# Optimization experiments

Hardware: AMD Instinct MI355X
Metric: run time of the kernel (lower is better)

## Reference

```python
import jax, jax.numpy as jnp
import numpy as np
import math

B, C, D, H, W = 1, 64, 16, 16, 16
HEADS = 4
HD = C // HEADS  # head_dim = 16


def conv3d(x, w, b, pad):
    # x: [B,C,D,H,W], w: [O,I,kd,kh,kw], pad: (pd,ph,pw)
    y = jax.lax.conv_general_dilated(
        x, w, window_strides=(1, 1, 1),
        padding=[(p, p) for p in pad],
        dimension_numbers=('NCDHW', 'OIDHW', 'NCDHW'))
    return y + b[None, :, None, None, None]


def setup_inputs() -> dict:
    key = jax.random.key(0)
    ks = jax.random.split(key, 10)
    s = 0.02
    return {
        'x': jax.random.normal(ks[0], (B, C, D, H, W), jnp.float32),
        'gamma': jax.random.normal(ks[1], (1,), jnp.float32),
        'w_sp': jax.random.normal(ks[2], (C, C, 1, 3, 3), jnp.float32) * s,
        'b_sp': jax.random.normal(ks[3], (C,), jnp.float32) * s,
        'w_spec': jax.random.normal(ks[4], (C, C, 3, 1, 1), jnp.float32) * s,
        'b_spec': jax.random.normal(ks[5], (C,), jnp.float32) * s,
        'w_qkv': jax.random.normal(ks[6], (3 * C, C, 1, 1, 1), jnp.float32) * s,
        'b_qkv': jax.random.normal(ks[7], (3 * C,), jnp.float32) * s,
        'w_proj': jax.random.normal(ks[8], (C, C, 1, 1, 1), jnp.float32) * s,
        'b_proj': jax.random.normal(ks[9], (C,), jnp.float32) * s,
    }


def _decay_exponent(dtype):
    # Faithful to the torch permute quirk (requires H == W):
    # exponent[i,j,k,m,n,o] = |i-m| + |j-k| + |n-o|
    dd = jnp.abs(jnp.arange(D)[:, None] - jnp.arange(D)[None, :]).astype(dtype)  # [D,D]
    hh = jnp.abs(jnp.arange(H)[:, None] - jnp.arange(H)[None, :]).astype(dtype)  # [H,H]
    ww = jnp.abs(jnp.arange(W)[:, None] - jnp.arange(W)[None, :]).astype(dtype)  # [W,W]
    return (dd[:, None, None, :, None, None]      # i (axis0), m (axis3)
            + hh[None, :, :, None, None, None]    # j (axis1), k (axis2)
            + ww[None, None, None, None, :, :])   # n (axis4), o (axis5)


def _forward(x, gamma, w_sp, b_sp, w_spec, b_spec, w_qkv, b_qkv, w_proj, b_proj):
    x = conv3d(x, w_sp, b_sp, (0, 1, 1))
    x = conv3d(x, w_spec, b_spec, (1, 0, 0))
    qkv = conv3d(x, w_qkv, b_qkv, (0, 0, 0))
    q, k, v = jnp.split(qkv, 3, axis=1)
    rs = lambda t: t.reshape(B, HEADS, HD, D, H, W)
    q, k, v = rs(q), rs(k), rs(v)

    g = jax.nn.sigmoid(gamma[0])
    decay = g ** _decay_exponent(x.dtype)  # [D,H,W,D,W,W] (H==W)

    # attn[b,h,i,j,k,m,n,o]: (i,j,k)=query D,H,W ; (m,n,o)=key D,H,W
    attn = jnp.einsum('bhdijk,bhdmno->bhijkmno', q, k) / math.sqrt(HD)
    attn = jax.nn.softmax(attn * decay, axis=-1)  # softmax over key-W axis o only
    out = jnp.einsum('bhijkmno,bhdmno->bhdijk', attn, v)
    out = out.reshape(B, C, D, H, W)
    return conv3d(out, w_proj, b_proj, (0, 0, 0))


def reference(x, gamma, w_sp, b_sp, w_spec, b_spec, w_qkv, b_qkv, w_proj, b_proj):
    return _forward(x, gamma, w_sp, b_sp, w_spec, b_spec, w_qkv, b_qkv, w_proj, b_proj)
```

## Files before the change

### kernel.cpp

```cpp
#include <hip/hip_runtime.h>
#include <math.h>

#define CN   262144
#define BTP 196
#define PTP 68

typedef __attribute__((ext_vector_type(8))) short short8;
typedef __attribute__((ext_vector_type(4))) short short4v;
typedef __attribute__((ext_vector_type(4))) float float4v;

static __device__ __forceinline__ unsigned short f2bf(float f) {
    union { float f; unsigned u; } v; v.f = f;
    unsigned r = (v.u + 0x7FFFu + ((v.u >> 16) & 1u)) >> 16;
    return (unsigned short)r;
}

__global__ __launch_bounds__(512) void wprep_kernel(
        const float* __restrict__ w_sp,
        const float* __restrict__ w_spec, const float* __restrict__ b_spec,
        const float* __restrict__ w_qkv, const float* __restrict__ b_qkv,
        unsigned short* __restrict__ wsb,
        unsigned short* __restrict__ wfb, float* __restrict__ bfv) {
    int idx = blockIdx.x * 512 + threadIdx.x;
    if (idx < 36864) {
        int dh  = idx / 12288;
        int rem = idx % 12288;
        int co  = rem / 192;
        int kp  = rem % 192;
        int ci = kp / 3, dw = kp % 3;
        wsb[idx] = f2bf(w_sp[co * 576 + ci * 9 + dh * 3 + dw]);
    } else {
        int j = idx - 36864;
        int oc = j / 192;
        int r  = j % 192;
        float s = 0.f;
        #pragma unroll 8
        for (int ci = 0; ci < 64; ++ci)
            s += w_qkv[oc * 64 + ci] * w_spec[ci * 192 + r];
        if (oc < 64) s *= 0.25f;
        wfb[oc * 192 + r] = f2bf(s);
        if (j < 192) {
            float t = b_qkv[j];
            for (int ci = 0; ci < 64; ++ci) t += w_qkv[j * 64 + ci] * b_spec[ci];
            if (j < 64) t *= 0.25f;
            bfv[j] = t;
        }
    }
}

__global__ __launch_bounds__(256, 4) void conv_sp_mfma_kernel(
        const float* __restrict__ x, const unsigned short* __restrict__ wsb,
        const float* __restrict__ b_sp, float* __restrict__ y1) {
    __shared__ __align__(16) unsigned short Bt[16 * BTP];
    int d = blockIdx.x >> 4;
    int h = blockIdx.x & 15;
    int tid = threadIdx.x;
    int px = tid & 15, cig = tid >> 4;

    float rcur[12], rnxt[12];
    #define LOAD_CHUNK(dh_, rr)                                            \
        {                                                                  \
            int hh = h + (dh_) - 1;                                        \
            _Pragma("unroll")                                              \
            for (int cc = 0; cc < 4; ++cc) {                               \
                int ci = cig * 4 + cc;                                     \
                const float* xr = x + ci * 4096 + d * 256 + hh * 16;       \
                _Pragma("unroll")                                          \
                for (int dw = 0; dw < 3; ++dw) {                           \
                    int ww = px + dw - 1;                                  \
                    float v = 0.f;                                         \
                    if (hh >= 0 && hh <= 15 && ww >= 0 && ww <= 15)        \
                        v = xr[ww];                                        \
                    (rr)[cc * 3 + dw] = v;                                 \
                }                                                          \
            }                                                              \
        }

    LOAD_CHUNK(0, rcur);

    int wv = tid >> 6, lane = tid & 63;
    int quad = lane >> 4, l15 = lane & 15;
    float4v czero = {0.f, 0.f, 0.f, 0.f};
    float4v acc = czero;

    #pragma unroll
    for (int c = 0; c < 3; ++c) {
        __syncthreads();
        #pragma unroll
        for (int cc = 0; cc < 4; ++cc) {
            int ci = cig * 4 + cc;
            Bt[px * BTP + ci * 3 + 0] = f2bf(rcur[cc * 3 + 0]);
            Bt[px * BTP + ci * 3 + 1] = f2bf(rcur[cc * 3 + 1]);
            Bt[px * BTP + ci * 3 + 2] = f2bf(rcur[cc * 3 + 2]);
        }
        __syncthreads();
        if (c < 2) LOAD_CHUNK(c + 1, rnxt);

        const unsigned short* ab = wsb + c * 12288 + (wv * 16 + l15) * 192 + quad * 8;
        const unsigned short* brow = Bt + l15 * BTP + quad * 8;
        #pragma unroll
        for (int ks = 0; ks < 6; ++ks) {
            short8 af = *(const short8*)(ab + ks * 32);
            short4v lo = *(const short4v*)(brow + ks * 32);
            short4v hi = *(const short4v*)(brow + ks * 32 + 4);
            short8 bf8 = {lo[0], lo[1], lo[2], lo[3], hi[0], hi[1], hi[2], hi[3]};
            acc = __builtin_amdgcn_mfma_f32_16x16x32_bf16(af, bf8, acc, 0, 0, 0);
        }
        #pragma unroll
        for (int q2 = 0; q2 < 12; ++q2) rcur[q2] = rnxt[q2];
    }

    int p = d * 256 + h * 16 + l15;
    #pragma unroll
    for (int r = 0; r < 4; ++r) {
        int co = wv * 16 + quad * 4 + r;
        y1[co * 4096 + p] = acc[r] + b_sp[co];
    }
    #undef LOAD_CHUNK
}

__global__ __launch_bounds__(512, 4) void qkv_mfma_kernel(
        const float* __restrict__ y1, const unsigned short* __restrict__ wfb,
        const float* __restrict__ bfv,
        unsigned short* __restrict__ qb, unsigned short* __restrict__ kb,
        unsigned short* __restrict__ vtb) {
    __shared__ __align__(16) unsigned short Bt[32 * BTP];
    int bI  = blockIdx.x;
    int ocg = bI % 3;
    int pq  = (bI / 3) & 7;
    int d   = bI / 24;
    int tid = threadIdx.x;

    {
        int px  = tid & 31;
        int cig = tid >> 5;
        const float* yb = y1 + d * 256 + pq * 32 + px;
        #pragma unroll
        for (int cc = 0; cc < 4; ++cc) {
            int ci = cig * 4 + cc;
            const float* yc = yb + ci * 4096;
            #pragma unroll
            for (int t = 0; t < 3; ++t) {
                float v = 0.f;
                if (!((d == 0 && t == 0) || (d == 15 && t == 2)))
                    v = yc[(t - 1) * 256];
                Bt[px * BTP + ci * 3 + t] = f2bf(v);
            }
        }
    }

    int wv = tid >> 6, lane = tid & 63;
    int quad = lane >> 4, l15 = lane & 15;
    int Mt = wv >> 1;
    int nt = wv & 1;

    short8 af[6];
    {
        const unsigned short* ab = wfb + (ocg * 64 + Mt * 16 + l15) * 192 + quad * 8;
        #pragma unroll
        for (int ks = 0; ks < 6; ++ks) af[ks] = *(const short8*)(ab + ks * 32);
    }
    float bias[4];
    #pragma unroll
    for (int r = 0; r < 4; ++r) bias[r] = bfv[ocg * 64 + Mt * 16 + quad * 4 + r];

    __syncthreads();

    float4v czero = {0.f, 0.f, 0.f, 0.f};
    float4v acc = czero;
    {
        const unsigned short* brow = Bt + (nt * 16 + l15) * BTP + quad * 8;
        #pragma unroll
        for (int ks = 0; ks < 6; ++ks) {
            short4v lo = *(const short4v*)(brow + ks * 32);
            short4v hi = *(const short4v*)(brow + ks * 32 + 4);
            short8 bf8 = {lo[0], lo[1], lo[2], lo[3], hi[0], hi[1], hi[2], hi[3]};
            acc = __builtin_amdgcn_mfma_f32_16x16x32_bf16(af[ks], bf8, acc, 0, 0, 0);
        }
    }

    {
        int p = d * 256 + pq * 32 + nt * 16 + l15;
        if (ocg == 2) {
            int h = (p >> 4) & 15, w0 = p & 15;
            int kap = 8 * (w0 >> 2) + 4 * (h & 1) + (w0 & 3);
            unsigned short* dst = vtb + ((Mt * 16 + d) * 8 + (h >> 1)) * 512
                                      + (quad * 4) * 32 + kap;
            #pragma unroll
            for (int r = 0; r < 4; ++r) dst[r * 32] = f2bf(acc[r] + bias[r]);
        } else {
            unsigned short* dst = (ocg == 0 ? qb : kb) + Mt * 65536 + p * 16 + quad * 4;
            unsigned t0 = (unsigned)f2bf(acc[0] + bias[0])
                        | ((unsigned)f2bf(acc[1] + bias[1]) << 16);
            unsigned t1 = (unsigned)f2bf(acc[2] + bias[2])
                        | ((unsigned)f2bf(acc[3] + bias[3]) << 16);
            *(unsigned*)dst = t0;
            *(unsigned*)(dst + 2) = t1;
        }
    }
}

__global__ __launch_bounds__(512, 4) void attn_kernel(
        const unsigned short* __restrict__ qb, const unsigned short* __restrict__ kb,
        const unsigned short* __restrict__ vtb, const float* __restrict__ gamma,
        float* __restrict__ aoall) {
    __shared__ __align__(16) unsigned short ksh[2][4096];
    __shared__ __align__(16) unsigned short vsh[2][4096];
    __shared__ float gp[32];
    int tid = threadIdx.x;
    int bI = blockIdx.x;
    int head = bI >> 8;
    int mg   = (bI >> 5) & 7;
    int oct  = bI & 31;

    if (tid < 32) {
        float g = 1.f / (1.f + __expf(-gamma[0]));
        gp[tid] = __powf(g, (float)tid);
    }

    int wv = tid >> 6, lane = tid & 63;
    int quad = lane >> 4, l15 = lane & 15;
    int t = oct * 8 + wv;
    int i = t >> 4, j = t & 15;

    short8 zero8 = {0, 0, 0, 0, 0, 0, 0, 0};
    float4v czero = {0.f, 0.f, 0.f, 0.f};
    short8 qf = zero8;
    if (quad < 2)
        qf = *(const short8*)(qb + head * 65536 + (t * 16 + l15) * 16 + quad * 8);

    const unsigned short* kbh = kb  + head * 65536 + mg * 2 * 4096;
    const unsigned short* vbh = vtb + head * 65536 + mg * 2 * 4096;
    float4 k0 = ((const float4*)kbh)[tid];
    float4 v0 = ((const float4*)vbh)[tid];
    float4 k1 = ((const float4*)(kbh + 4096))[tid];
    float4 v1 = ((const float4*)(vbh + 4096))[tid];
    ((float4*)ksh[0])[tid] = k0;
    ((float4*)vsh[0])[tid] = v0;
    ((float4*)ksh[1])[tid] = k1;
    ((float4*)vsh[1])[tid] = v1;
    __syncthreads();

    float wd[4];
    #pragma unroll
    for (int r = 0; r < 4; ++r)
        wd[r] = gp[abs(l15 - (quad * 4 + r))] * 1.4426950408889634f;

    float4v O = czero;
    #pragma unroll
    for (int mm = 0; mm < 2; ++mm) {
        int m = mg * 2 + mm;
        const unsigned short* kk = ksh[mm];
        const unsigned short* vv = vsh[mm];
        int eim = abs(i - m);
        #pragma unroll
        for (int np = 0; np < 8; ++np) {
            union { unsigned u[4]; short8 s8; } a2u;
            #pragma unroll
            for (int s = 0; s < 2; ++s) {
                int n = np * 2 + s;
                short8 a1 = zero8;
                if (quad < 2)
                    a1 = *(const short8*)(kk + n * 256 + l15 * 16 + quad * 8);
                float4v d1 = __builtin_amdgcn_mfma_f32_16x16x32_bf16(a1, qf, czero, 0, 0, 0);
                float smn = gp[eim + abs(j - n)];
                float e0 = __builtin_amdgcn_exp2f(d1[0] * smn * wd[0]);
                float e1 = __builtin_amdgcn_exp2f(d1[1] * smn * wd[1]);
                float e2 = __builtin_amdgcn_exp2f(d1[2] * smn * wd[2]);
                float e3 = __builtin_amdgcn_exp2f(d1[3] * smn * wd[3]);
                float sm = e0 + e1 + e2 + e3;
                sm += __shfl_xor(sm, 16);
                sm += __shfl_xor(sm, 32);
                float inv = __builtin_amdgcn_rcpf(sm);
                union { float f; unsigned u; } p0, p1, p2, p3;
                p0.f = e0 * inv; p1.f = e1 * inv;
                p2.f = e2 * inv; p3.f = e3 * inv;
                a2u.u[s * 2]     = ((p0.u + 0x8000u) >> 16) | ((p1.u + 0x8000u) & 0xFFFF0000u);
                a2u.u[s * 2 + 1] = ((p2.u + 0x8000u) >> 16) | ((p3.u + 0x8000u) & 0xFFFF0000u);
            }
            short8 b2 = *(const short8*)(vv + np * 512 + l15 * 32 + quad * 8);
            O = __builtin_amdgcn_mfma_f32_16x16x32_bf16(a2u.s8, b2, O, 0, 0, 0);
        }
    }

    float* aop = aoall + mg * CN;
    float4 ov = {O[0], O[1], O[2], O[3]};
    *(float4*)(aop + (head * 16 + l15) * 4096 + t * 16 + quad * 4) = ov;
}

__global__ __launch_bounds__(256, 8) void proj_mfma_kernel(
        const float* __restrict__ aoall,
        const float* __restrict__ w, const float* __restrict__ b,
        float* __restrict__ out) {
    __shared__ __align__(16) unsigned short Bt[16 * PTP];
    int d   = blockIdx.x >> 4;
    int p16 = blockIdx.x & 15;
    int tid = threadIdx.x;

    {
        int px = tid & 15, cig = tid >> 4;
        int gbase = d * 256 + p16 * 16 + px;
        #pragma unroll
        for (int cc = 0; cc < 4; ++cc) {
            int ci = cig * 4 + cc;
            int ga = ci * 4096 + gbase;
            float v = 0.f;
            #pragma unroll
            for (int k = 0; k < 8; ++k) v += aoall[k * CN + ga];
            Bt[px * PTP + ci] = f2bf(v);
        }
    }
    __syncthreads();

    int wv = tid >> 6, lane = tid & 63;
    int quad = lane >> 4, l15 = lane & 15;
    float4v czero = {0.f, 0.f, 0.f, 0.f};
    float4v acc = czero;

    short8 af[2];
    const float* wsrc = w + (wv * 16 + l15) * 64 + quad * 8;
    #pragma unroll
    for (int ks = 0; ks < 2; ++ks) {
        float4 wa = *(const float4*)(wsrc + ks * 32);
        float4 wb = *(const float4*)(wsrc + ks * 32 + 4);
        short8 a8 = {(short)f2bf(wa.x), (short)f2bf(wa.y), (short)f2bf(wa.z),
                     (short)f2bf(wa.w), (short)f2bf(wb.x), (short)f2bf(wb.y),
                     (short)f2bf(wb.z), (short)f2bf(wb.w)};
        af[ks] = a8;
    }
    const unsigned short* brow = Bt + l15 * PTP + quad * 8;
    #pragma unroll
    for (int ks = 0; ks < 2; ++ks) {
        short4v lo = *(const short4v*)(brow + ks * 32);
        short4v hi = *(const short4v*)(brow + ks * 32 + 4);
        short8 bf8 = {lo[0], lo[1], lo[2], lo[3], hi[0], hi[1], hi[2], hi[3]};
        acc = __builtin_amdgcn_mfma_f32_16x16x32_bf16(af[ks], bf8, acc, 0, 0, 0);
    }

    int p = d * 256 + p16 * 16 + l15;
    #pragma unroll
    for (int r = 0; r < 4; ++r) {
        int oc = wv * 16 + quad * 4 + r;
        out[oc * 4096 + p] = acc[r] + b[oc];
    }
}

extern "C" void kernel_launch(void* const* d_in, const int* in_sizes, int n_in,
                              void* d_out, int out_size, void* d_ws, size_t ws_size,
                              hipStream_t stream) {
    const float* x      = (const float*)d_in[0];
    const float* gamma  = (const float*)d_in[1];
    const float* w_sp   = (const float*)d_in[2];
    const float* b_sp   = (const float*)d_in[3];
    const float* w_spec = (const float*)d_in[4];
    const float* b_spec = (const float*)d_in[5];
    const float* w_qkv  = (const float*)d_in[6];
    const float* b_qkv  = (const float*)d_in[7];
    const float* w_proj = (const float*)d_in[8];
    const float* b_proj = (const float*)d_in[9];
    float* out = (float*)d_out;

    float* ws = (float*)d_ws;
    float* y1  = ws;
    unsigned short* wfb = (unsigned short*)(ws + CN);
    float* bfv = ws + CN + 20480;
    unsigned short* wsb = (unsigned short*)(ws + CN + 24576);
    unsigned short* qb  = (unsigned short*)(ws + 2 * CN);
    unsigned short* kb  = (unsigned short*)(ws + 2 * CN + CN / 2);
    unsigned short* vtb = (unsigned short*)(ws + 3 * CN);
    float* aoall = ws + 3 * CN + CN / 2;

    wprep_kernel       <<< 144, 512, 0, stream>>>(w_sp, w_spec, b_spec,
                                                  w_qkv, b_qkv, wsb, wfb, bfv);
    conv_sp_mfma_kernel<<< 256, 256, 0, stream>>>(x, wsb, b_sp, y1);
    qkv_mfma_kernel    <<< 384, 512, 0, stream>>>(y1, wfb, bfv, qb, kb, vtb);
    attn_kernel        <<<1024, 512, 0, stream>>>(qb, kb, vtb, gamma, aoall);
    proj_mfma_kernel   <<< 256, 256, 0, stream>>>(aoall, w_proj, b_proj, out);
}
```

Baseline: 117.2 us.

## Fuse all five stages into one persistent kernel with grid barriers

Replaces the five separate kernel launches (weight prep, spatial conv, qkv, attention, projection) with a single persistent kernel of 512 blocks. The stages are separated by atomic-counter grid barriers, and the barrier counter is reset with a memset before each launch. The aim is to remove per-launch overhead and the idle gaps between dependent kernels. The cost is spin-wait barrier overhead and underused blocks in the smaller stages. Correctness also relies on all 512 blocks being co-resident, since the spin waits are only guarded by an iteration cap.

```diff
diff --git a/kernel.cpp b/kernel.cpp
--- a/kernel.cpp
+++ b/kernel.cpp
@@ -15,333 +15,367 @@
     return (unsigned short)r;
 }
 
-__global__ __launch_bounds__(512) void wprep_kernel(
-        const float* __restrict__ w_sp,
+static __device__ __forceinline__ void grid_bar(int* bar, int target) {
+    __syncthreads();
+    if (threadIdx.x == 0) {
+        __threadfence();
+        atomicAdd(bar, 1);
+        int z = 0;
+        while (__hip_atomic_load(bar, __ATOMIC_RELAXED, __HIP_MEMORY_SCOPE_AGENT) < target
+               && z < (1 << 22)) {
+            __builtin_amdgcn_s_sleep(1);
+            ++z;
+        }
+        __threadfence();
+    }
+    __syncthreads();
+}
+
+__global__ __launch_bounds__(512, 4) void mega_kernel(
+        const float* __restrict__ x, const float* __restrict__ gamma,
+        const float* __restrict__ w_sp, const float* __restrict__ b_sp,
         const float* __restrict__ w_spec, const float* __restrict__ b_spec,
         const float* __restrict__ w_qkv, const float* __restrict__ b_qkv,
-        unsigned short* __restrict__ wsb,
-        unsigned short* __restrict__ wfb, float* __restrict__ bfv) {
-    int idx = blockIdx.x * 512 + threadIdx.x;
-    if (idx < 36864) {
-        int dh  = idx / 12288;
-        int rem = idx % 12288;
-        int co  = rem / 192;
-        int kp  = rem % 192;
-        int ci = kp / 3, dw = kp % 3;
-        wsb[idx] = f2bf(w_sp[co * 576 + ci * 9 + dh * 3 + dw]);
-    } else {
-        int j = idx - 36864;
-        int oc = j / 192;
-        int r  = j % 192;
-        float s = 0.f;
-        #pragma unroll 8
-        for (int ci = 0; ci < 64; ++ci)
-            s += w_qkv[oc * 64 + ci] * w_spec[ci * 192 + r];
-        if (oc < 64) s *= 0.25f;
-        wfb[oc * 192 + r] = f2bf(s);
-        if (j < 192) {
-            float t = b_qkv[j];
-            for (int ci = 0; ci < 64; ++ci) t += w_qkv[j * 64 + ci] * b_spec[ci];
-            if (j < 64) t *= 0.25f;
-            bfv[j] = t;
-        }
-    }
-}
-
-__global__ __launch_bounds__(256, 4) void conv_sp_mfma_kernel(
-        const float* __restrict__ x, const unsigned short* __restrict__ wsb,
-        const float* __restrict__ b_sp, float* __restrict__ y1) {
-    __shared__ __align__(16) unsigned short Bt[16 * BTP];
-    int d = blockIdx.x >> 4;
-    int h = blockIdx.x & 15;
-    int tid = threadIdx.x;
-    int px = tid & 15, cig = tid >> 4;
-
-    float rcur[12], rnxt[12];
-    #define LOAD_CHUNK(dh_, rr)                                            \
-        {                                                                  \
-            int hh = h + (dh_) - 1;                                        \
-            _Pragma("unroll")                                              \
-            for (int cc = 0; cc < 4; ++cc) {                               \
-                int ci = cig * 4 + cc;                                     \
-                const float* xr = x + ci * 4096 + d * 256 + hh * 16;       \
-                _Pragma("unroll")                                          \
-                for (int dw = 0; dw < 3; ++dw) {                           \
-                    int ww = px + dw - 1;                                  \
-                    float v = 0.f;                                         \
-                    if (hh >= 0 && hh <= 15 && ww >= 0 && ww <= 15)        \
-                        v = xr[ww];                                        \
-                    (rr)[cc * 3 + dw] = v;                                 \
-                }                                                          \
-            }                                                              \
-        }
-
-    LOAD_CHUNK(0, rcur);
-
-    int wv = tid >> 6, lane = tid & 63;
-    int quad = lane >> 4, l15 = lane & 15;
-    float4v czero = {0.f, 0.f, 0.f, 0.f};
-    float4v acc = czero;
-
-    #pragma unroll
-    for (int c = 0; c < 3; ++c) {
+        const float* __restrict__ w_proj, const float* __restrict__ b_proj,
+        float* __restrict__ out, float* ws, int* bar) {
+    __shared__ __align__(16) unsigned char lds_raw[32896];
+
+    float* y1  = ws;
+    unsigned short* wfb = (unsigned short*)(ws + CN);
+    float* bfv = ws + CN + 20480;
+    unsigned short* wsb = (unsigned short*)(ws + CN + 24576);
+    unsigned short* qb  = (unsigned short*)(ws + 2 * CN);
+    unsigned short* kb  = (unsigned short*)(ws + 2 * CN + CN / 2);
+    unsigned short* vtb = (unsigned short*)(ws + 3 * CN);
+    float* aoall = ws + 3 * CN + CN / 2;
+
+    {
+        int idx = blockIdx.x * 512 + threadIdx.x;
+        if (idx < 36864) {
+            int dh  = idx / 12288;
+            int rem = idx % 12288;
+            int co  = rem / 192;
+            int kp  = rem % 192;
+            int ci = kp / 3, dw = kp % 3;
+            wsb[idx] = f2bf(w_sp[co * 576 + ci * 9 + dh * 3 + dw]);
+        } else if (idx < 73728) {
+            int j = idx - 36864;
+            int oc = j / 192;
+            int r  = j % 192;
+            float s = 0.f;
+            #pragma unroll 8
+            for (int ci = 0; ci < 64; ++ci)
+                s += w_qkv[oc * 64 + ci] * w_spec[ci * 192 + r];
+            if (oc < 64) s *= 0.25f;
+            wfb[oc * 192 + r] = f2bf(s);
+            if (j < 192) {
+                float t = b_qkv[j];
+                for (int ci = 0; ci < 64; ++ci) t += w_qkv[j * 64 + ci] * b_spec[ci];
+                if (j < 64) t *= 0.25f;
+                bfv[j] = t;
+            }
+        }
+    }
+    grid_bar(bar, 512);
+
+    if (blockIdx.x < 256) {
+        unsigned short* Bt = (unsigned short*)lds_raw;
+        int d = blockIdx.x >> 4;
+        int h = blockIdx.x & 15;
+        int tid = threadIdx.x;
+        bool act = tid < 256;
+        int px = tid & 15, cig = (tid >> 4) & 15;
+
+        float rcur[12], rnxt[12];
+        #define LOAD_CHUNK(dh_, rr)                                            \
+            {                                                                  \
+                int hh = h + (dh_) - 1;                                        \
+                _Pragma("unroll")                                              \
+                for (int cc = 0; cc < 4; ++cc) {                               \
+                    int ci = cig * 4 + cc;                                     \
+                    const float* xr = x + ci * 4096 + d * 256 + hh * 16;       \
+                    _Pragma("unroll")                                          \
+                    for (int dw = 0; dw < 3; ++dw) {                           \
+                        int ww = px + dw - 1;                                  \
+                        float v = 0.f;                                         \
+                        if (hh >= 0 && hh <= 15 && ww >= 0 && ww <= 15)        \
+                            v = xr[ww];                                        \
+                        (rr)[cc * 3 + dw] = v;                                 \
+                    }                                                          \
+                }                                                              \
+            }
+
+        if (act) LOAD_CHUNK(0, rcur);
+
+        int wv = (tid >> 6) & 3, lane = tid & 63;
+        int quad = lane >> 4, l15 = lane & 15;
+        float4v acc = {0.f, 0.f, 0.f, 0.f};
+
+        #pragma unroll
+        for (int c = 0; c < 3; ++c) {
+            __syncthreads();
+            if (act) {
+                #pragma unroll
+                for (int cc = 0; cc < 4; ++cc) {
+                    int ci = cig * 4 + cc;
+                    Bt[px * BTP + ci * 3 + 0] = f2bf(rcur[cc * 3 + 0]);
+                    Bt[px * BTP + ci * 3 + 1] = f2bf(rcur[cc * 3 + 1]);
+                    Bt[px * BTP + ci * 3 + 2] = f2bf(rcur[cc * 3 + 2]);
+                }
+            }
+            __syncthreads();
+            if (act) {
+                if (c < 2) LOAD_CHUNK(c + 1, rnxt);
+
+                const unsigned short* ab = wsb + c * 12288 + (wv * 16 + l15) * 192 + quad * 8;
+                const unsigned short* brow = Bt + l15 * BTP + quad * 8;
+                #pragma unroll
+                for (int ks = 0; ks < 6; ++ks) {
+                    short8 af = *(const short8*)(ab + ks * 32);
+                    short4v lo = *(const short4v*)(brow + ks * 32);
+                    short4v hi = *(const short4v*)(brow + ks * 32 + 4);
+                    short8 bf8 = {lo[0], lo[1], lo[2], lo[3], hi[0], hi[1], hi[2], hi[3]};
+                    acc = __builtin_amdgcn_mfma_f32_16x16x32_bf16(af, bf8, acc, 0, 0, 0);
+                }
+                #pragma unroll
+                for (int q2 = 0; q2 < 12; ++q2) rcur[q2] = rnxt[q2];
+            }
+        }
+
+        if (act) {
+            int p = d * 256 + h * 16 + l15;
+            #pragma unroll
+            for (int r = 0; r < 4; ++r) {
+                int co = wv * 16 + quad * 4 + r;
+                y1[co * 4096 + p] = acc[r] + b_sp[co];
+            }
+        }
+        #undef LOAD_CHUNK
+    }
+    grid_bar(bar, 1024);
+
+    if (blockIdx.x < 384) {
+        unsigned short* Bt = (unsigned short*)lds_raw;
+        int bI  = blockIdx.x;
+        int ocg = bI % 3;
+        int pq  = (bI / 3) & 7;
+        int d   = bI / 24;
+        int tid = threadIdx.x;
+
+        {
+            int px  = tid & 31;
+            int cig = tid >> 5;
+            const float* yb = y1 + d * 256 + pq * 32 + px;
+            #pragma unroll
+            for (int cc = 0; cc < 4; ++cc) {
+                int ci = cig * 4 + cc;
+                const float* yc = yb + ci * 4096;
+                #pragma unroll
+                for (int t = 0; t < 3; ++t) {
+                    float v = 0.f;
+                    if (!((d == 0 && t == 0) || (d == 15 && t == 2)))
+                        v = yc[(t - 1) * 256];
+                    Bt[px * BTP + ci * 3 + t] = f2bf(v);
+                }
+            }
+        }
+
+        int wv = tid >> 6, lane = tid & 63;
+        int quad = lane >> 4, l15 = lane & 15;
+        int Mt = wv >> 1;
+        int nt = wv & 1;
+
+        short8 af[6];
+        {
+            const unsigned short* ab = wfb + (ocg * 64 + Mt * 16 + l15) * 192 + quad * 8;
+            #pragma unroll
+            for (int ks = 0; ks < 6; ++ks) af[ks] = *(const short8*)(ab + ks * 32);
+        }
+        float bias[4];
+        #pragma unroll
+        for (int r = 0; r < 4; ++r) bias[r] = bfv[ocg * 64 + Mt * 16 + quad * 4 + r];
+
         __syncthreads();
-        #pragma unroll
-        for (int cc = 0; cc < 4; ++cc) {
-            int ci = cig * 4 + cc;
-            Bt[px * BTP + ci * 3 + 0] = f2bf(rcur[cc * 3 + 0]);
-            Bt[px * BTP + ci * 3 + 1] = f2bf(rcur[cc * 3 + 1]);
-            Bt[px * BTP + ci * 3 + 2] = f2bf(rcur[cc * 3 + 2]);
+
+        float4v czero = {0.f, 0.f, 0.f, 0.f};
+        float4v acc = czero;
+        {
+            const unsigned short* brow = Bt + (nt * 16 + l15) * BTP + quad * 8;
+            #pragma unroll
+            for (int ks = 0; ks < 6; ++ks) {
+                short4v lo = *(const short4v*)(brow + ks * 32);
+                short4v hi = *(const short4v*)(brow + ks * 32 + 4);
+                short8 bf8 = {lo[0], lo[1], lo[2], lo[3], hi[0], hi[1], hi[2], hi[3]};
+                acc = __builtin_amdgcn_mfma_f32_16x16x32_bf16(af[ks], bf8, acc, 0, 0, 0);
+            }
+        }
+
+        {
+            int p = d * 256 + pq * 32 + nt * 16 + l15;
+            if (ocg == 2) {
+                int h = (p >> 4) & 15, w0 = p & 15;
+                int kap = 8 * (w0 >> 2) + 4 * (h & 1) + (w0 & 3);
+                unsigned short* dst = vtb + ((Mt * 16 + d) * 8 + (h >> 1)) * 512
+                                          + (quad * 4) * 32 + kap;
+                #pragma unroll
+                for (int r = 0; r < 4; ++r) dst[r * 32] = f2bf(acc[r] + bias[r]);
+            } else {
+                unsigned short* dst = (ocg == 0 ? qb : kb) + Mt * 65536 + p * 16 + quad * 4;
+                unsigned t0 = (unsigned)f2bf(acc[0] + bias[0])
+                            | ((unsigned)f2bf(acc[1] + bias[1]) << 16);
+                unsigned t1 = (unsigned)f2bf(acc[2] + bias[2])
+                            | ((unsigned)f2bf(acc[3] + bias[3]) << 16);
+                *(unsigned*)dst = t0;
+                *(unsigned*)(dst + 2) = t1;
+            }
+        }
+    }
+    grid_bar(bar, 1536);
+
+    {
+        unsigned short* KSH = (unsigned short*)lds_raw;
+        unsigned short* VSH = (unsigned short*)lds_raw + 8192;
+        float* gp = (float*)(lds_raw + 32768);
+        int tid = threadIdx.x;
+        if (tid < 32) {
+            float g = 1.f / (1.f + __expf(-gamma[0]));
+            gp[tid] = __powf(g, (float)tid);
+        }
+        int wv = tid >> 6, lane = tid & 63;
+        int quad = lane >> 4, l15 = lane & 15;
+        short8 zero8 = {0, 0, 0, 0, 0, 0, 0, 0};
+        float4v czero = {0.f, 0.f, 0.f, 0.f};
+
+        #pragma unroll 1
+        for (int it = 0; it < 2; ++it) {
+            int bI = blockIdx.x + it * 512;
+            int head = bI >> 8;
+            int mg   = (bI >> 5) & 7;
+            int oct  = bI & 31;
+            int t = oct * 8 + wv;
+            int i = t >> 4, j = t & 15;
+
+            short8 qf = zero8;
+            if (quad < 2)
+                qf = *(const short8*)(qb + head * 65536 + (t * 16 + l15) * 16 + quad * 8);
+
+            const unsigned short* kbh = kb  + head * 65536 + mg * 2 * 4096;
+            const unsigned short* vbh = vtb + head * 65536 + mg * 2 * 4096;
+            float4 k0 = ((const float4*)kbh)[tid];
+            float4 v0 = ((const float4*)vbh)[tid];
+            float4 k1 = ((const float4*)(kbh + 4096))[tid];
+            float4 v1 = ((const float4*)(vbh + 4096))[tid];
+            __syncthreads();
+            ((float4*)KSH)[tid] = k0;
+            ((float4*)VSH)[tid] = v0;
+            ((float4*)(KSH + 4096))[tid] = k1;
+            ((float4*)(VSH + 4096))[tid] = v1;
+            __syncthreads();
+
+            float wd[4];
+            #pragma unroll
+            for (int r = 0; r < 4; ++r)
+                wd[r] = gp[abs(l15 - (quad * 4 + r))] * 1.4426950408889634f;
+
+            float4v O = czero;
+            #pragma unroll
+            for (int mm = 0; mm < 2; ++mm) {
+                int m = mg * 2 + mm;
+                const unsigned short* kk = KSH + mm * 4096;
+                const unsigned short* vv = VSH + mm * 4096;
+                int eim = abs(i - m);
+                #pragma unroll
+                for (int np = 0; np < 8; ++np) {
+                    union { unsigned u[4]; short8 s8; } a2u;
+                    #pragma unroll
+                    for (int s = 0; s < 2; ++s) {
+                        int n = np * 2 + s;
+                        short8 a1 = zero8;
+                        if (quad < 2)
+                            a1 = *(const short8*)(kk + n * 256 + l15 * 16 + quad * 8);
+                        float4v d1 = __builtin_amdgcn_mfma_f32_16x16x32_bf16(a1, qf, czero, 0, 0, 0);
+                        float smn = gp[eim + abs(j - n)];
+                        float e0 = __builtin_amdgcn_exp2f(d1[0] * smn * wd[0]);
+                        float e1 = __builtin_amdgcn_exp2f(d1[1] * smn * wd[1]);
+                        float e2 = __builtin_amdgcn_exp2f(d1[2] * smn * wd[2]);
+                        float e3 = __builtin_amdgcn_exp2f(d1[3] * smn * wd[3]);
+                        float sm = e0 + e1 + e2 + e3;
+                        sm += __shfl_xor(sm, 16);
+                        sm += __shfl_xor(sm, 32);
+                        float inv = __builtin_amdgcn_rcpf(sm);
+                        union { float f; unsigned u; } p0, p1, p2, p3;
+                        p0.f = e0 * inv; p1.f = e1 * inv;
+                        p2.f = e2 * inv; p3.f = e3 * inv;
+                        a2u.u[s * 2]     = ((p0.u + 0x8000u) >> 16) | ((p1.u + 0x8000u) & 0xFFFF0000u);
+                        a2u.u[s * 2 + 1] = ((p2.u + 0x8000u) >> 16) | ((p3.u + 0x8000u) & 0xFFFF0000u);
+                    }
+                    short8 b2 = *(const short8*)(vv + np * 512 + l15 * 32 + quad * 8);
+                    O = __builtin_amdgcn_mfma_f32_16x16x32_bf16(a2u.s8, b2, O, 0, 0, 0);
+                }
+            }
+
+            float* aop = aoall + mg * CN;
+            float4 ov = {O[0], O[1], O[2], O[3]};
+            *(float4*)(aop + (head * 16 + l15) * 4096 + t * 16 + quad * 4) = ov;
+        }
+    }
+    grid_bar(bar, 2048);
+
+    if (blockIdx.x < 256) {
+        unsigned short* Bt = (unsigned short*)lds_raw;
+        int d   = blockIdx.x >> 4;
+        int p16 = blockIdx.x & 15;
+        int tid = threadIdx.x;
+        bool act = tid < 256;
+
+        if (act) {
+            int px = tid & 15, cig = (tid >> 4) & 15;
+            int gbase = d * 256 + p16 * 16 + px;
+            #pragma unroll
+            for (int cc = 0; cc < 4; ++cc) {
+                int ci = cig * 4 + cc;
+                int ga = ci * 4096 + gbase;
+                float v = 0.f;
+                #pragma unroll
+                for (int k = 0; k < 8; ++k) v += aoall[k * CN + ga];
+                Bt[px * PTP + ci] = f2bf(v);
+            }
         }
         __syncthreads();
-        if (c < 2) LOAD_CHUNK(c + 1, rnxt);
-
-        const unsigned short* ab = wsb + c * 12288 + (wv * 16 + l15) * 192 + quad * 8;
-        const unsigned short* brow = Bt + l15 * BTP + quad * 8;
-        #pragma unroll
-        for (int ks = 0; ks < 6; ++ks) {
-            short8 af = *(const short8*)(ab + ks * 32);
-            short4v lo = *(const short4v*)(brow + ks * 32);
-            short4v hi = *(const short4v*)(brow + ks * 32 + 4);
-            short8 bf8 = {lo[0], lo[1], lo[2], lo[3], hi[0], hi[1], hi[2], hi[3]};
-            acc = __builtin_amdgcn_mfma_f32_16x16x32_bf16(af, bf8, acc, 0, 0, 0);
-        }
-        #pragma unroll
-        for (int q2 = 0; q2 < 12; ++q2) rcur[q2] = rnxt[q2];
-    }
-
-    int p = d * 256 + h * 16 + l15;
-    #pragma unroll
-    for (int r = 0; r < 4; ++r) {
-        int co = wv * 16 + quad * 4 + r;
-        y1[co * 4096 + p] = acc[r] + b_sp[co];
-    }
-    #undef LOAD_CHUNK
-}
-
-__global__ __launch_bounds__(512, 4) void qkv_mfma_kernel(
-        const float* __restrict__ y1, const unsigned short* __restrict__ wfb,
-        const float* __restrict__ bfv,
-        unsigned short* __restrict__ qb, unsigned short* __restrict__ kb,
-        unsigned short* __restrict__ vtb) {
-    __shared__ __align__(16) unsigned short Bt[32 * BTP];
-    int bI  = blockIdx.x;
-    int ocg = bI % 3;
-    int pq  = (bI / 3) & 7;
-    int d   = bI / 24;
-    int tid = threadIdx.x;
-
-    {
-        int px  = tid & 31;
-        int cig = tid >> 5;
-        const float* yb = y1 + d * 256 + pq * 32 + px;
-        #pragma unroll
-        for (int cc = 0; cc < 4; ++cc) {
-            int ci = cig * 4 + cc;
-            const float* yc = yb + ci * 4096;
-            #pragma unroll
-            for (int t = 0; t < 3; ++t) {
-                float v = 0.f;
-                if (!((d == 0 && t == 0) || (d == 15 && t == 2)))
-                    v = yc[(t - 1) * 256];
-                Bt[px * BTP + ci * 3 + t] = f2bf(v);
-            }
-        }
-    }
-
-    int wv = tid >> 6, lane = tid & 63;
-    int quad = lane >> 4, l15 = lane & 15;
-    int Mt = wv >> 1;
-    int nt = wv & 1;
-
-    short8 af[6];
-    {
-        const unsigned short* ab = wfb + (ocg * 64 + Mt * 16 + l15) * 192 + quad * 8;
-        #pragma unroll
-        for (int ks = 0; ks < 6; ++ks) af[ks] = *(const short8*)(ab + ks * 32);
-    }
-    float bias[4];
-    #pragma unroll
-    for (int r = 0; r < 4; ++r) bias[r] = bfv[ocg * 64 + Mt * 16 + quad * 4 + r];
-
-    __syncthreads();
-
-    float4v czero = {0.f, 0.f, 0.f, 0.f};
-    float4v acc = czero;
-    {
-        const unsigned short* brow = Bt + (nt * 16 + l15) * BTP + quad * 8;
-        #pragma unroll
-        for (int ks = 0; ks < 6; ++ks) {
-            short4v lo = *(const short4v*)(brow + ks * 32);
-            short4v hi = *(const short4v*)(brow + ks * 32 + 4);
-            short8 bf8 = {lo[0], lo[1], lo[2], lo[3], hi[0], hi[1], hi[2], hi[3]};
-            acc = __builtin_amdgcn_mfma_f32_16x16x32_bf16(af[ks], bf8, acc, 0, 0, 0);
-        }
-    }
-
-    {
-        int p = d * 256 + pq * 32 + nt * 16 + l15;
-        if (ocg == 2) {
-            int h = (p >> 4) & 15, w0 = p & 15;
-            int kap = 8 * (w0 >> 2) + 4 * (h & 1) + (w0 & 3);
-            unsigned short* dst = vtb + ((Mt * 16 + d) * 8 + (h >> 1)) * 512
-                                      + (quad * 4) * 32 + kap;
-            #pragma unroll
-            for (int r = 0; r < 4; ++r) dst[r * 32] = f2bf(acc[r] + bias[r]);
-        } else {
-            unsigned short* dst = (ocg == 0 ? qb : kb) + Mt * 65536 + p * 16 + quad * 4;
-            unsigned t0 = (unsigned)f2bf(acc[0] + bias[0])
-                        | ((unsigned)f2bf(acc[1] + bias[1]) << 16);
-            unsigned t1 = (unsigned)f2bf(acc[2] + bias[2])
-                        | ((unsigned)f2bf(acc[3] + bias[3]) << 16);
-            *(unsigned*)dst = t0;
-            *(unsigned*)(dst + 2) = t1;
-        }
-    }
-}
-
-__global__ __launch_bounds__(512, 4) void attn_kernel(
-        const unsigned short* __restrict__ qb, const unsigned short* __restrict__ kb,
-        const unsigned short* __restrict__ vtb, const float* __restrict__ gamma,
-        float* __restrict__ aoall) {
-    __shared__ __align__(16) unsigned short ksh[2][4096];
-    __shared__ __align__(16) unsigned short vsh[2][4096];
-    __shared__ float gp[32];
-    int tid = threadIdx.x;
-    int bI = blockIdx.x;
-    int head = bI >> 8;
-    int mg   = (bI >> 5) & 7;
-    int oct  = bI & 31;
-
-    if (tid < 32) {
-        float g = 1.f / (1.f + __expf(-gamma[0]));
-        gp[tid] = __powf(g, (float)tid);
-    }
-
-    int wv = tid >> 6, lane = tid & 63;
-    int quad = lane >> 4, l15 = lane & 15;
-    int t = oct * 8 + wv;
-    int i = t >> 4, j = t & 15;
-
-    short8 zero8 = {0, 0, 0, 0, 0, 0, 0, 0};
-    float4v czero = {0.f, 0.f, 0.f, 0.f};
-    short8 qf = zero8;
-    if (quad < 2)
-        qf = *(const short8*)(qb + head * 65536 + (t * 16 + l15) * 16 + quad * 8);
-
-    const unsigned short* kbh = kb  + head * 65536 + mg * 2 * 4096;
-    const unsigned short* vbh = vtb + head * 65536 + mg * 2 * 4096;
-    float4 k0 = ((const float4*)kbh)[tid];
-    float4 v0 = ((const float4*)vbh)[tid];
-    float4 k1 = ((const float4*)(kbh + 4096))[tid];
-    float4 v1 = ((const float4*)(vbh + 4096))[tid];
-    ((float4*)ksh[0])[tid] = k0;
-    ((float4*)vsh[0])[tid] = v0;
-    ((float4*)ksh[1])[tid] = k1;
-    ((float4*)vsh[1])[tid] = v1;
-    __syncthreads();
-
-    float wd[4];
-    #pragma unroll
-    for (int r = 0; r < 4; ++r)
-        wd[r] = gp[abs(l15 - (quad * 4 + r))] * 1.4426950408889634f;
-
-    float4v O = czero;
-    #pragma unroll
-    for (int mm = 0; mm < 2; ++mm) {
-        int m = mg * 2 + mm;
-        const unsigned short* kk = ksh[mm];
-        const unsigned short* vv = vsh[mm];
-        int eim = abs(i - m);
-        #pragma unroll
-        for (int np = 0; np < 8; ++np) {
-            union { unsigned u[4]; short8 s8; } a2u;
-            #pragma unroll
-            for (int s = 0; s < 2; ++s) {
-                int n = np * 2 + s;
-                short8 a1 = zero8;
-                if (quad < 2)
-                    a1 = *(const short8*)(kk + n * 256 + l15 * 16 + quad * 8);
-                float4v d1 = __builtin_amdgcn_mfma_f32_16x16x32_bf16(a1, qf, czero, 0, 0, 0);
-                float smn = gp[eim + abs(j - n)];
-                float e0 = __builtin_amdgcn_exp2f(d1[0] * smn * wd[0]);
-                float e1 = __builtin_amdgcn_exp2f(d1[1] * smn * wd[1]);
-                float e2 = __builtin_amdgcn_exp2f(d1[2] * smn * wd[2]);
-                float e3 = __builtin_amdgcn_exp2f(d1[3] * smn * wd[3]);
-                float sm = e0 + e1 + e2 + e3;
-                sm += __shfl_xor(sm, 16);
-                sm += __shfl_xor(sm, 32);
-                float inv = __builtin_amdgcn_rcpf(sm);
-                union { float f; unsigned u; } p0, p1, p2, p3;
-                p0.f = e0 * inv; p1.f = e1 * inv;
-                p2.f = e2 * inv; p3.f = e3 * inv;
-                a2u.u[s * 2]     = ((p0.u + 0x8000u) >> 16) | ((p1.u + 0x8000u) & 0xFFFF0000u);
-                a2u.u[s * 2 + 1] = ((p2.u + 0x8000u) >> 16) | ((p3.u + 0x8000u) & 0xFFFF0000u);
-            }
-            short8 b2 = *(const short8*)(vv + np * 512 + l15 * 32 + quad * 8);
-            O = __builtin_amdgcn_mfma_f32_16x16x32_bf16(a2u.s8, b2, O, 0, 0, 0);
-        }
-    }
-
-    float* aop = aoall + mg * CN;
-    float4 ov = {O[0], O[1], O[2], O[3]};
-    *(float4*)(aop + (head * 16 + l15) * 4096 + t * 16 + quad * 4) = ov;
-}
-
-__global__ __launch_bounds__(256, 8) void proj_mfma_kernel(
-        const float* __restrict__ aoall,
-        const float* __restrict__ w, const float* __restrict__ b,
-        float* __restrict__ out) {
-    __shared__ __align__(16) unsigned short Bt[16 * PTP];
-    int d   = blockIdx.x >> 4;
-    int p16 = blockIdx.x & 15;
-    int tid = threadIdx.x;
-
-    {
-        int px = tid & 15, cig = tid >> 4;
-        int gbase = d * 256 + p16 * 16 + px;
-        #pragma unroll
-        for (int cc = 0; cc < 4; ++cc) {
-            int ci = cig * 4 + cc;
-            int ga = ci * 4096 + gbase;
-            float v = 0.f;
-            #pragma unroll
-            for (int k = 0; k < 8; ++k) v += aoall[k * CN + ga];
-            Bt[px * PTP + ci] = f2bf(v);
-        }
-    }
-    __syncthreads();
-
-    int wv = tid >> 6, lane = tid & 63;
-    int quad = lane >> 4, l15 = lane & 15;
-    float4v czero = {0.f, 0.f, 0.f, 0.f};
-    float4v acc = czero;
-
-    short8 af[2];
-    const float* wsrc = w + (wv * 16 + l15) * 64 + quad * 8;
-    #pragma unroll
-    for (int ks = 0; ks < 2; ++ks) {
-        float4 wa = *(const float4*)(wsrc + ks * 32);
-        float4 wb = *(const float4*)(wsrc + ks * 32 + 4);
-        short8 a8 = {(short)f2bf(wa.x), (short)f2bf(wa.y), (short)f2bf(wa.z),
-                     (short)f2bf(wa.w), (short)f2bf(wb.x), (short)f2bf(wb.y),
-                     (short)f2bf(wb.z), (short)f2bf(wb.w)};
-        af[ks] = a8;
-    }
-    const unsigned short* brow = Bt + l15 * PTP + quad * 8;
-    #pragma unroll
-    for (int ks = 0; ks < 2; ++ks) {
-        short4v lo = *(const short4v*)(brow + ks * 32);
-        short4v hi = *(const short4v*)(brow + ks * 32 + 4);
-        short8 bf8 = {lo[0], lo[1], lo[2], lo[3], hi[0], hi[1], hi[2], hi[3]};
-        acc = __builtin_amdgcn_mfma_f32_16x16x32_bf16(af[ks], bf8, acc, 0, 0, 0);
-    }
-
-    int p = d * 256 + p16 * 16 + l15;
-    #pragma unroll
-    for (int r = 0; r < 4; ++r) {
-        int oc = wv * 16 + quad * 4 + r;
-        out[oc * 4096 + p] = acc[r] + b[oc];
+
+        if (act) {
+            int wv = (tid >> 6) & 3, lane = tid & 63;
+            int quad = lane >> 4, l15 = lane & 15;
+            float4v czero = {0.f, 0.f, 0.f, 0.f};
+            float4v acc = czero;
+
+            short8 af[2];
+            const float* wsrc = w_proj + (wv * 16 + l15) * 64 + quad * 8;
+            #pragma unroll
+            for (int ks = 0; ks < 2; ++ks) {
+                float4 wa = *(const float4*)(wsrc + ks * 32);
+                float4 wb = *(const float4*)(wsrc + ks * 32 + 4);
+                short8 a8 = {(short)f2bf(wa.x), (short)f2bf(wa.y), (short)f2bf(wa.z),
+                             (short)f2bf(wa.w), (short)f2bf(wb.x), (short)f2bf(wb.y),
+                             (short)f2bf(wb.z), (short)f2bf(wb.w)};
+                af[ks] = a8;
+            }
+            const unsigned short* brow = Bt + l15 * PTP + quad * 8;
+            #pragma unroll
+            for (int ks = 0; ks < 2; ++ks) {
+                short4v lo = *(const short4v*)(brow + ks * 32);
+                short4v hi = *(const short4v*)(brow + ks * 32 + 4);
+                short8 bf8 = {lo[0], lo[1], lo[2], lo[3], hi[0], hi[1], hi[2], hi[3]};
+                acc = __builtin_amdgcn_mfma_f32_16x16x32_bf16(af[ks], bf8, acc, 0, 0, 0);
+            }
+
+            int p = d * 256 + p16 * 16 + l15;
+            #pragma unroll
+            for (int r = 0; r < 4; ++r) {
+                int oc = wv * 16 + quad * 4 + r;
+                out[oc * 4096 + p] = acc[r] + b_proj[oc];
+            }
+        }
     }
 }
 
@@ -359,21 +393,12 @@
     const float* w_proj = (const float*)d_in[8];
     const float* b_proj = (const float*)d_in[9];
     float* out = (float*)d_out;
-
     float* ws = (float*)d_ws;
-    float* y1  = ws;
-    unsigned short* wfb = (unsigned short*)(ws + CN);
-    float* bfv = ws + CN + 20480;
-    unsigned short* wsb = (unsigned short*)(ws + CN + 24576);
-    unsigned short* qb  = (unsigned short*)(ws + 2 * CN);
-    unsigned short* kb  = (unsigned short*)(ws + 2 * CN + CN / 2);
-    unsigned short* vtb = (unsigned short*)(ws + 3 * CN);
-    float* aoall = ws + 3 * CN + CN / 2;
-
-    wprep_kernel       <<< 144, 512, 0, stream>>>(w_sp, w_spec, b_spec,
-                                                  w_qkv, b_qkv, wsb, wfb, bfv);
-    conv_sp_mfma_kernel<<< 256, 256, 0, stream>>>(x, wsb, b_sp, y1);
-    qkv_mfma_kernel    <<< 384, 512, 0, stream>>>(y1, wfb, bfv, qb, kb, vtb);
-    attn_kernel        <<<1024, 512, 0, stream>>>(qb, kb, vtb, gamma, aoall);
-    proj_mfma_kernel   <<< 256, 256, 0, stream>>>(aoall, w_proj, b_proj, out);
+
+    int* bar = (int*)(ws + 12 * CN);
+    hipMemsetAsync(bar, 0, 256, stream);
+
+    mega_kernel<<<dim3(512), dim3(512), 0, stream>>>(
+        x, gamma, w_sp, b_sp, w_spec, b_spec, w_qkv, b_qkv, w_proj, b_proj,
+        out, ws, bar);
 }
```

Result: slower. 291.7 us (+148.9%).
